# Optimization experiments

Hardware: AMD Instinct MI355X
Metric: run time of the kernel (lower is better)

## Reference

```python
import jax, jax.numpy as jnp
import numpy as np

B, N, E, FIN, FOUT = 4, 50000, 800000, 128, 64
ALPHA = 0.2  # LeakyReLU negative slope
NEG_BIG = -9e15


def setup_inputs() -> dict:
    key = jax.random.key(0)
    kx, kw, ka, ksrc, kdst = jax.random.split(key, 5)
    X = jax.random.normal(kx, (B, N, FIN), dtype=jnp.float32)
    W = jax.random.normal(kw, (FIN, FOUT), dtype=jnp.float32) * 0.1
    a = jax.random.normal(ka, (1, 2 * FOUT), dtype=jnp.float32) * 0.1
    # edges [B,2,E]; guarantee every row (destination of aggregation) has >=1 edge
    # so e_rowsum > 0 (mirrors real adjacency which has self-loops / connectivity).
    src_rand = jax.random.randint(ksrc, (B, E - N), 0, N, dtype=jnp.int32)
    src = jnp.concatenate(
        [jnp.broadcast_to(jnp.arange(N, dtype=jnp.int32), (B, N)), src_rand], axis=1
    )
    dst = jax.random.randint(kdst, (B, E), 0, N, dtype=jnp.int32)
    edges = jnp.stack([src, dst], axis=1)  # [B,2,E]
    return {"X": X, "edges": edges, "W": W, "a": a}


def _per_graph(x, edge, W, a):
    # x: [N,FIN], edge: [2,E]
    h = x @ W                                   # [N,FOUT]
    a1, a2 = a[0, :FOUT], a[0, FOUT:]           # split a . concat(h_i,h_j)
    s = (h @ a1)[edge[0]] + (h @ a2)[edge[1]]   # [E] attention logits
    edge_e = jnp.exp(-jax.nn.leaky_relu(s, ALPHA))          # [E]
    rowsum = jax.ops.segment_sum(edge_e, edge[0], num_segments=N)  # [N]
    msg = edge_e[:, None] * h[edge[1]]          # [E,FOUT]
    h_prime = jax.ops.segment_sum(msg, edge[0], num_segments=N)    # [N,FOUT]
    h_prime = h_prime / rowsum[:, None]
    h_prime = jnp.where(jnp.isnan(h_prime), jnp.float32(NEG_BIG), h_prime)
    return h_prime


def reference(X, edges, W, a):
    out = jax.vmap(_per_graph, in_axes=(0, 0, None, None))(X, edges, W, a)  # [B,N,FOUT]
    return jax.nn.elu(out)  # concat=True path
```

## Files before the change

### kernel.cpp

```cpp
#include <hip/hip_runtime.h>

#define B_    4
#define N_    50000
#define E_    800000
#define FIN_  128
#define F_    64
#define BN_   (B_ * N_)
#define TOT_  (BN_ * F_)
#define BE_   (B_ * E_)
#define ALPHA_ 0.2f
#define NEG_BIG_ -9.0e15f

#define XS_STRIDE 132
#define GEMM_BLOCKS (BN_ / 64)
#define COUNT_BLOCKS (BE_ / 1024)

__device__ __forceinline__ float bf2f(unsigned int u16) {
    union { unsigned int i; float f; } v;
    v.i = u16 << 16;
    return v.f;
}
__device__ __forceinline__ unsigned int f2bf(float f) {
    union { float f; unsigned int u; } v;
    v.f = f;
    unsigned int r = v.u + 0x7FFFu + ((v.u >> 16) & 1u);
    return r >> 16;
}

__global__ __launch_bounds__(256) void gemm_count_kernel(
    const float* __restrict__ X,
    const float* __restrict__ W,
    const float* __restrict__ a,
    const int* __restrict__ edges,
    unsigned short* __restrict__ hq,
    float* __restrict__ e1,
    float* __restrict__ e2,
    int* __restrict__ cnt,
    unsigned short* __restrict__ rank) {
    __shared__ float Wf[FIN_ * F_];
    __shared__ float Xs[64 * XS_STRIDE];

    const int tid = threadIdx.x;
    const int bid = blockIdx.x;

    if (bid & 1) {
        const int g  = (bid >> 1) * 256 + tid;
        const int ge = g * 4;
        const int b  = ge / E_;
        const int e  = ge - b * E_;
        const int4 s4 = *(const int4*)&edges[(size_t)b * 2 * E_ + e];
        ushort4 r4;
        r4.x = (unsigned short)atomicAdd(&cnt[b * N_ + s4.x], 1);
        r4.y = (unsigned short)atomicAdd(&cnt[b * N_ + s4.y], 1);
        r4.z = (unsigned short)atomicAdd(&cnt[b * N_ + s4.z], 1);
        r4.w = (unsigned short)atomicAdd(&cnt[b * N_ + s4.w], 1);
        *(ushort4*)&rank[ge] = r4;
        return;
    }

    const float4* Wg = (const float4*)W;
    for (int i = tid; i < 2048; i += 256)
        ((float4*)Wf)[i] = Wg[i];

    const int row0 = (bid >> 1) * 64;
    const float4* Xg = (const float4*)(X + (size_t)row0 * FIN_);
    for (int i = tid; i < 2048; i += 256) {
        const int r = i >> 5;
        const int c = i & 31;
        float4 v = Xg[i];
        *(float4*)&Xs[r * XS_STRIDE + c * 4] = v;
    }
    __syncthreads();

    const int cg = tid & 15;
    const int rg = tid >> 4;

    float acc[4][4] = {};
#pragma unroll 4
    for (int k = 0; k < FIN_; ++k) {
        const float4 wv = *(const float4*)&Wf[k * F_ + cg * 4];
        float xr[4];
#pragma unroll
        for (int j = 0; j < 4; ++j)
            xr[j] = Xs[(rg * 4 + j) * XS_STRIDE + k];
#pragma unroll
        for (int j = 0; j < 4; ++j) {
            acc[j][0] += xr[j] * wv.x;
            acc[j][1] += xr[j] * wv.y;
            acc[j][2] += xr[j] * wv.z;
            acc[j][3] += xr[j] * wv.w;
        }
    }

    float a1v[4], a2v[4];
#pragma unroll
    for (int i = 0; i < 4; ++i) {
        a1v[i] = a[cg * 4 + i];
        a2v[i] = a[F_ + cg * 4 + i];
    }

#pragma unroll
    for (int j = 0; j < 4; ++j) {
        const int row = row0 + rg * 4 + j;
        union { ushort4 v; unsigned short s[4]; } st;
#pragma unroll
        for (int i = 0; i < 4; ++i) st.s[i] = (unsigned short)f2bf(acc[j][i]);
        *(ushort4*)&hq[(size_t)row * F_ + cg * 4] = st.v;

        float p1 = acc[j][0] * a1v[0] + acc[j][1] * a1v[1] +
                   acc[j][2] * a1v[2] + acc[j][3] * a1v[3];
        float p2 = acc[j][0] * a2v[0] + acc[j][1] * a2v[1] +
                   acc[j][2] * a2v[2] + acc[j][3] * a2v[3];
#pragma unroll
        for (int m = 8; m >= 1; m >>= 1) {
            p1 += __shfl_xor(p1, m);
            p2 += __shfl_xor(p2, m);
        }
        if (cg == 0) { e1[row] = p1; e2[row] = p2; }
    }
}

#define SB_ 196
#define SE_ 1024

__global__ __launch_bounds__(256) void scanA_kernel(
    const int* __restrict__ cnt, int* __restrict__ bsum) {
    __shared__ int red[256];
    const int t = threadIdx.x;
    const int base = blockIdx.x * SE_ + t * 4;
    int s = 0;
    if (base < BN_) {
        const int4 v = *(const int4*)&cnt[base];
        s = v.x + v.y + v.z + v.w;
    }
    red[t] = s;
    __syncthreads();
    for (int off = 128; off >= 1; off >>= 1) {
        if (t < off) red[t] += red[t + off];
        __syncthreads();
    }
    if (t == 0) bsum[blockIdx.x] = red[0];
}

__global__ __launch_bounds__(256) void scanB_kernel(
    const int* __restrict__ bsum, int* __restrict__ boff,
    int* __restrict__ offs) {
    __shared__ int s[256];
    const int t = threadIdx.x;
    const int v = (t < SB_) ? bsum[t] : 0;
    s[t] = v;
    __syncthreads();
    for (int off = 1; off < 256; off <<= 1) {
        const int u = (t >= off) ? s[t - off] : 0;
        __syncthreads();
        s[t] += u;
        __syncthreads();
    }
    if (t < SB_) boff[t] = s[t] - v;
    if (t == SB_ - 1) offs[BN_] = s[t];
}

__global__ __launch_bounds__(256) void scanC_kernel(
    const int* __restrict__ cnt, const int* __restrict__ boff,
    int* __restrict__ offs) {
    __shared__ int s[256];
    const int t = threadIdx.x;
    const int base = blockIdx.x * SE_ + t * 4;
    int4 v = make_int4(0, 0, 0, 0);
    if (base < BN_) v = *(const int4*)&cnt[base];
    const int tot = v.x + v.y + v.z + v.w;
    s[t] = tot;
    __syncthreads();
    for (int off = 1; off < 256; off <<= 1) {
        const int u = (t >= off) ? s[t - off] : 0;
        __syncthreads();
        s[t] += u;
        __syncthreads();
    }
    if (base < BN_) {
        int run = boff[blockIdx.x] + s[t] - tot;
        int4 o;
        o.x = run;
        o.y = run + v.x;
        o.z = o.y + v.y;
        o.w = o.z + v.z;
        *(int4*)&offs[base] = o;
    }
}

__global__ __launch_bounds__(256) void place_kernel(
    const int* __restrict__ edges,
    const float* __restrict__ e1,
    const float* __restrict__ e2,
    const int* __restrict__ offs,
    const unsigned short* __restrict__ rank,
    unsigned int* __restrict__ csr) {
    const int g  = blockIdx.x * 256 + threadIdx.x;
    const int ge = g * 4;
    const int b  = ge / E_;
    const int e  = ge - b * E_;
    const int4 s4 = *(const int4*)&edges[(size_t)b * 2 * E_ + e];
    const int4 d4 = *(const int4*)&edges[(size_t)b * 2 * E_ + E_ + e];
    const ushort4 r4 = *(const ushort4*)&rank[ge];
    const int ss[4] = { s4.x, s4.y, s4.z, s4.w };
    const int dd[4] = { d4.x, d4.y, d4.z, d4.w };
    const int rr[4] = { r4.x, r4.y, r4.z, r4.w };
#pragma unroll
    for (int j = 0; j < 4; ++j) {
        const int gs = b * N_ + ss[j];
        const float sv = e1[gs] + e2[b * N_ + dd[j]];
        const float lr = sv > 0.0f ? sv : ALPHA_ * sv;
        const float wt = __expf(-lr);
        csr[offs[gs] + rr[j]] = (unsigned int)dd[j] | (f2bf(wt) << 16);
    }
}

__global__ __launch_bounds__(256) void gather_kernel(
    const int* __restrict__ offs,
    const unsigned int* __restrict__ csr,
    const uint2* __restrict__ hq2,
    float* __restrict__ out) {
    const int lane = threadIdx.x & 63;
    const int grp = lane >> 4;
    const int sub = lane & 15;
    const int gs = (int)((blockIdx.x * 256 + threadIdx.x) >> 6);
    const int b = gs / N_;
    const uint2* hb = hq2 + (size_t)b * N_ * 16;
    const int k0 = offs[gs];
    const int k1 = offs[gs + 1];

    float a0 = 0.0f, a1 = 0.0f, a2 = 0.0f, a3 = 0.0f, rs = 0.0f;

    int k = k0 + grp;
    unsigned int e_cur = 0u, e_nxt = 0u;
    uint2 p_cur = make_uint2(0u, 0u);
    if (k < k1) e_cur = csr[k];
    if (k + 4 < k1) e_nxt = csr[k + 4];
    if (k < k1) p_cur = hb[(size_t)(e_cur & 0xFFFFu) * 16 + sub];

    for (; k < k1; k += 4) {
        uint2 p_nxt = make_uint2(0u, 0u);
        if (k + 4 < k1) p_nxt = hb[(size_t)(e_nxt & 0xFFFFu) * 16 + sub];
        unsigned int e_nn = 0u;
        if (k + 8 < k1) e_nn = csr[k + 8];

        const float wt = bf2f(e_cur >> 16);
        a0 += wt * bf2f(p_cur.x & 0xFFFFu);
        a1 += wt * bf2f(p_cur.x >> 16);
        a2 += wt * bf2f(p_cur.y & 0xFFFFu);
        a3 += wt * bf2f(p_cur.y >> 16);
        rs += wt;

        e_cur = e_nxt; e_nxt = e_nn; p_cur = p_nxt;
    }

    a0 += __shfl_xor(a0, 16); a1 += __shfl_xor(a1, 16);
    a2 += __shfl_xor(a2, 16); a3 += __shfl_xor(a3, 16);
    rs += __shfl_xor(rs, 16);
    a0 += __shfl_xor(a0, 32); a1 += __shfl_xor(a1, 32);
    a2 += __shfl_xor(a2, 32); a3 += __shfl_xor(a3, 32);
    rs += __shfl_xor(rs, 32);

    if (grp == 0) {
        float v[4];
        v[0] = a0 / rs; v[1] = a1 / rs; v[2] = a2 / rs; v[3] = a3 / rs;
        float4 o;
        float* po = (float*)&o;
#pragma unroll
        for (int j = 0; j < 4; ++j) {
            float x = v[j];
            if (x != x) x = NEG_BIG_;
            po[j] = x > 0.0f ? x : (__expf(x) - 1.0f);
        }
        *(float4*)&out[(size_t)gs * F_ + sub * 4] = o;
    }
}

extern "C" void kernel_launch(void* const* d_in, const int* in_sizes, int n_in,
                              void* d_out, int out_size, void* d_ws, size_t ws_size,
                              hipStream_t stream) {
    const float* X = (const float*)d_in[0];
    const int* edges = (const int*)d_in[1];
    const float* W = (const float*)d_in[2];
    const float* a = (const float*)d_in[3];
    float* out = (float*)d_out;

    float* e1 = (float*)d_ws;
    float* e2 = e1 + BN_;
    unsigned short* hq = (unsigned short*)(e2 + BN_);
    int* cnt = (int*)(hq + (size_t)BN_ * F_);
    int* offs = cnt + BN_;
    unsigned short* rank = (unsigned short*)(offs + BN_ + 4);
    unsigned int* csr = (unsigned int*)(rank + BE_);
    int* bsum = (int*)(csr + BE_);
    int* boff = bsum + 256;

    hipMemsetAsync(cnt, 0, (size_t)BN_ * sizeof(int), stream);

    gemm_count_kernel<<<GEMM_BLOCKS + COUNT_BLOCKS, 256, 0, stream>>>(
        X, W, a, edges, hq, e1, e2, cnt, rank);
    scanA_kernel<<<SB_, 256, 0, stream>>>(cnt, bsum);
    scanB_kernel<<<1, 256, 0, stream>>>(bsum, boff, offs);
    scanC_kernel<<<SB_, 256, 0, stream>>>(cnt, boff, offs);
    place_kernel<<<BE_ / 1024, 256, 0, stream>>>(edges, e1, e2, offs, rank, csr);
    gather_kernel<<<BN_ / 4, 256, 0, stream>>>(offs, csr, (const uint2*)hq, out);
}
```

Before: 435.2 us.

## Pipeline per-graph CSR placement with gather of previous graph in fused launches

```diff
diff --git a/kernel.cpp b/kernel.cpp
--- a/kernel.cpp
+++ b/kernel.cpp
@@ -14,6 +14,9 @@
 #define XS_STRIDE 132
 #define GEMM_BLOCKS (BN_ / 64)
 #define COUNT_BLOCKS (BE_ / 1024)
+
+#define PL_BLOCKS 782
+#define GA_BLOCKS (N_ / 4)
 
 __device__ __forceinline__ float bf2f(unsigned int u16) {
     union { unsigned int i; float f; } v;
@@ -188,44 +191,44 @@
     }
 }
 
-__global__ __launch_bounds__(256) void place_kernel(
+__device__ __forceinline__ void place_body(
+    int pb, int blk, int tid,
     const int* __restrict__ edges,
     const float* __restrict__ e1,
     const float* __restrict__ e2,
     const int* __restrict__ offs,
     const unsigned short* __restrict__ rank,
     unsigned int* __restrict__ csr) {
-    const int g  = blockIdx.x * 256 + threadIdx.x;
-    const int ge = g * 4;
-    const int b  = ge / E_;
-    const int e  = ge - b * E_;
-    const int4 s4 = *(const int4*)&edges[(size_t)b * 2 * E_ + e];
-    const int4 d4 = *(const int4*)&edges[(size_t)b * 2 * E_ + E_ + e];
-    const ushort4 r4 = *(const ushort4*)&rank[ge];
+    const int e = (blk * 256 + tid) * 4;
+    if (e >= E_) return;
+    const int4 s4 = *(const int4*)&edges[(size_t)pb * 2 * E_ + e];
+    const int4 d4 = *(const int4*)&edges[(size_t)pb * 2 * E_ + E_ + e];
+    const ushort4 r4 = *(const ushort4*)&rank[(size_t)pb * E_ + e];
     const int ss[4] = { s4.x, s4.y, s4.z, s4.w };
     const int dd[4] = { d4.x, d4.y, d4.z, d4.w };
     const int rr[4] = { r4.x, r4.y, r4.z, r4.w };
 #pragma unroll
     for (int j = 0; j < 4; ++j) {
-        const int gs = b * N_ + ss[j];
-        const float sv = e1[gs] + e2[b * N_ + dd[j]];
+        const int gs = pb * N_ + ss[j];
+        const float sv = e1[gs] + e2[pb * N_ + dd[j]];
         const float lr = sv > 0.0f ? sv : ALPHA_ * sv;
         const float wt = __expf(-lr);
         csr[offs[gs] + rr[j]] = (unsigned int)dd[j] | (f2bf(wt) << 16);
     }
 }
 
-__global__ __launch_bounds__(256) void gather_kernel(
+__device__ __forceinline__ void gather_body(
+    int gb, int blk, int tid,
     const int* __restrict__ offs,
     const unsigned int* __restrict__ csr,
     const uint2* __restrict__ hq2,
     float* __restrict__ out) {
-    const int lane = threadIdx.x & 63;
+    const int lane = tid & 63;
     const int grp = lane >> 4;
     const int sub = lane & 15;
-    const int gs = (int)((blockIdx.x * 256 + threadIdx.x) >> 6);
-    const int b = gs / N_;
-    const uint2* hb = hq2 + (size_t)b * N_ * 16;
+    const int s = (int)((blk * 256 + tid) >> 6);
+    const int gs = gb * N_ + s;
+    const uint2* hb = hq2 + (size_t)gb * N_ * 16;
     const int k0 = offs[gs];
     const int k1 = offs[gs + 1];
 
@@ -274,6 +277,28 @@
         }
         *(float4*)&out[(size_t)gs * F_ + sub * 4] = o;
     }
+}
+
+__global__ __launch_bounds__(256) void place_gather_kernel(
+    const int* __restrict__ edges,
+    const float* __restrict__ e1,
+    const float* __restrict__ e2,
+    const int* __restrict__ offs,
+    const unsigned short* __restrict__ rank,
+    unsigned int* __restrict__ csr,
+    const uint2* __restrict__ hq2,
+    float* __restrict__ out,
+    int pb, int gb) {
+    const int tid = threadIdx.x;
+    int bid = blockIdx.x;
+    if (pb >= 0) {
+        if (bid < PL_BLOCKS) {
+            place_body(pb, bid, tid, edges, e1, e2, offs, rank, csr);
+            return;
+        }
+        bid -= PL_BLOCKS;
+    }
+    gather_body(gb, bid, tid, offs, csr, hq2, out);
 }
 
 extern "C" void kernel_launch(void* const* d_in, const int* in_sizes, int n_in,
@@ -295,13 +320,20 @@
     int* bsum = (int*)(csr + BE_);
     int* boff = bsum + 256;
 
-    hipMemsetAsync(cnt, 0, (size_t)BN_ * sizeof(int), stream);
+    (void)hipMemsetAsync(cnt, 0, (size_t)BN_ * sizeof(int), stream);
 
     gemm_count_kernel<<<GEMM_BLOCKS + COUNT_BLOCKS, 256, 0, stream>>>(
         X, W, a, edges, hq, e1, e2, cnt, rank);
     scanA_kernel<<<SB_, 256, 0, stream>>>(cnt, bsum);
     scanB_kernel<<<1, 256, 0, stream>>>(bsum, boff, offs);
     scanC_kernel<<<SB_, 256, 0, stream>>>(cnt, boff, offs);
-    place_kernel<<<BE_ / 1024, 256, 0, stream>>>(edges, e1, e2, offs, rank, csr);
-    gather_kernel<<<BN_ / 4, 256, 0, stream>>>(offs, csr, (const uint2*)hq, out);
-}
+
+    const uint2* hq2 = (const uint2*)hq;
+    place_gather_kernel<<<PL_BLOCKS, 256, 0, stream>>>(
+        edges, e1, e2, offs, rank, csr, hq2, out, 0, -1);
+    for (int b = 0; b < B_ - 1; ++b)
+        place_gather_kernel<<<PL_BLOCKS + GA_BLOCKS, 256, 0, stream>>>(
+            edges, e1, e2, offs, rank, csr, hq2, out, b + 1, b);
+    place_gather_kernel<<<GA_BLOCKS, 256, 0, stream>>>(
+        edges, e1, e2, offs, rank, csr, hq2, out, -1, B_ - 1);
+}
```

Result: no change. 437.4 us (+0.5%).
